# Kernel tuning notes

Hardware: AMD Instinct MI355X
Metric: run time of the kernel (lower is better)

The kernel has to match this reference:

```python
import jax, jax.numpy as jnp
import numpy as np

EPS = 1e-6
NUM_HEADS = 16


def _layer_norm(x, alpha, beta):
    # Custom LN: unbiased std, divides by (std + eps) -- matches source exactly.
    mean = jnp.mean(x, axis=-1, keepdims=True)
    std = jnp.std(x, axis=-1, keepdims=True, ddof=1)
    return alpha * (x - mean) / (std + EPS) + beta


def _mha(x, wq, bq, wk, bk, wv, bv, wo, bo):
    B, S, D = x.shape
    H = NUM_HEADS
    Dh = D // H
    q = (x @ wq.T + bq).reshape(B, S, H, Dh)
    k = (x @ wk.T + bk).reshape(B, S, H, Dh)
    v = (x @ wv.T + bv).reshape(B, S, H, Dh)
    scores = jnp.einsum('bqhd,bkhd->bhqk', q, k) / jnp.sqrt(jnp.float32(Dh)).astype(x.dtype)
    p = jax.nn.softmax(scores, axis=-1)
    out = jnp.einsum('bhqk,bkhd->bqhd', p, v).reshape(B, S, D)
    return out @ wo.T + bo


def _ffn(x, w1, b1, w2, b2):
    return jax.nn.relu(x @ w1.T + b1) @ w2.T + b2


def setup_inputs() -> dict:
    key = jax.random.key(0)
    ks = jax.random.split(key, 8)
    B, S, D, Hf = 8, 1024, 1024, 4096
    s = lambda d: 1.0 / np.sqrt(d)
    return {
        'x': jax.random.normal(ks[0], (B, S, D), jnp.float32),
        'src_mask': jnp.ones((B, 1, 1, S), jnp.int32),
        'wq': jax.random.normal(ks[1], (D, D), jnp.float32) * s(D),
        'bq': jnp.zeros((D,), jnp.float32),
        'wk': jax.random.normal(ks[2], (D, D), jnp.float32) * s(D),
        'bk': jnp.zeros((D,), jnp.float32),
        'wv': jax.random.normal(ks[3], (D, D), jnp.float32) * s(D),
        'bv': jnp.zeros((D,), jnp.float32),
        'wo': jax.random.normal(ks[4], (D, D), jnp.float32) * s(D),
        'bo': jnp.zeros((D,), jnp.float32),
        'w1': jax.random.normal(ks[5], (Hf, D), jnp.float32) * s(D),
        'b1': jnp.zeros((Hf,), jnp.float32),
        'w2': jax.random.normal(ks[6], (D, Hf), jnp.float32) * s(Hf),
        'b2': jnp.zeros((D,), jnp.float32),
        'alpha': jnp.ones((D,), jnp.float32),
        'beta': jnp.zeros((D,), jnp.float32),
    }


def reference(x, src_mask, wq, bq, wk, bk, wv, bv, wo, bo, w1, b1, w2, b2, alpha, beta):
    # src_mask is unused in the source's attention implementation (faithful).
    # Pre-LN residual block 1: attention (shared LN params alpha/beta).
    x = x + _mha(_layer_norm(x, alpha, beta), wq, bq, wk, bk, wv, bv, wo, bo)
    # Pre-LN residual block 2: feed-forward (same shared LN instance).
    x = x + _ffn(_layer_norm(x, alpha, beta), w1, b1, w2, b2)
    return x
```

## Files before the change

### kernel.cpp

```cpp
#include <hip/hip_runtime.h>
#include <hip/hip_bf16.h>
#include <stdint.h>

typedef __bf16 bf16;
typedef __attribute__((ext_vector_type(8))) __bf16 bf16x8;
typedef __attribute__((ext_vector_type(4))) __bf16 bf16x4;
typedef __attribute__((ext_vector_type(4))) float floatx4;

typedef __attribute__((address_space(3))) uint32_t* lds_u32p;
typedef const __attribute__((address_space(1))) uint32_t* glb_u32p;

__device__ __forceinline__ void gload16(void* lds, const void* g) {
  __builtin_amdgcn_global_load_lds((glb_u32p)(uintptr_t)g,
                                   (lds_u32p)(uintptr_t)lds, 16, 0, 0);
}

__global__ __launch_bounds__(256) void detect_kernel(
    const unsigned short* __restrict__ xr, int* __restrict__ flag) {
  __shared__ int cnt;
  if (threadIdx.x == 0) cnt = 0;
  __syncthreads();
  int c = 0;
  for (int i = threadIdx.x; i < 8192; i += 256) {
    unsigned short e = (xr[i] >> 7) & 0xFF;
    if (e >= 0x90) ++c;
  }
  atomicAdd(&cnt, c);
  __syncthreads();
  if (threadIdx.x == 0) *flag = (cnt > 64) ? 1 : 0;
}

#define NCONV 14
struct ConvArgs {
  const void* src[NCONV];
  bf16* dst[NCONV];
  int nelem[NCONV];
  int bstart[NCONV + 1];
};

__global__ __launch_bounds__(256) void convert_kernel(ConvArgs a, const int* __restrict__ flag) {
  const int isf = *flag;
  const int bx = blockIdx.x;
  int t = 0;
  #pragma unroll
  for (int i = 1; i < NCONV; ++i)
    if (bx >= a.bstart[i]) t = i;
  const int base = (bx - a.bstart[t]) * 2048 + threadIdx.x * 8;
  if (base >= a.nelem[t]) return;
  if (isf) {
    const float* s = (const float*)a.src[t] + base;
    const float4 x0 = *reinterpret_cast<const float4*>(s);
    const float4 x1 = *reinterpret_cast<const float4*>(s + 4);
    bf16x8 o;
    o[0] = (bf16)x0.x; o[1] = (bf16)x0.y; o[2] = (bf16)x0.z; o[3] = (bf16)x0.w;
    o[4] = (bf16)x1.x; o[5] = (bf16)x1.y; o[6] = (bf16)x1.z; o[7] = (bf16)x1.w;
    *reinterpret_cast<bf16x8*>(a.dst[t] + base) = o;
  } else {
    *reinterpret_cast<bf16x8*>(a.dst[t] + base) =
        *reinterpret_cast<const bf16x8*>((const bf16*)a.src[t] + base);
  }
}

__global__ __launch_bounds__(256) void ln_kernel(
    const void* __restrict__ x, const bf16* __restrict__ alpha,
    const bf16* __restrict__ beta, bf16* __restrict__ y,
    const int* __restrict__ flag, int x_ext) {
  const int isf = *flag;
  const int row = blockIdx.x;
  const int tid = threadIdx.x;

  float v0, v1, v2, v3;
  if (x_ext && isf) {
    const float4 xv = *reinterpret_cast<const float4*>(
        (const float*)x + (size_t)row * 1024 + tid * 4);
    v0 = xv.x; v1 = xv.y; v2 = xv.z; v3 = xv.w;
  } else {
    const bf16x4 xv = *reinterpret_cast<const bf16x4*>(
        (const bf16*)x + (size_t)row * 1024 + tid * 4);
    v0 = (float)xv[0]; v1 = (float)xv[1]; v2 = (float)xv[2]; v3 = (float)xv[3];
  }
  float s = v0 + v1 + v2 + v3;
  float ss = v0 * v0 + v1 * v1 + v2 * v2 + v3 * v3;
  #pragma unroll
  for (int off = 32; off > 0; off >>= 1) {
    s += __shfl_down(s, off);
    ss += __shfl_down(ss, off);
  }
  __shared__ float red[8];
  __shared__ float s_mean, s_inv;
  const int w = tid >> 6, lane = tid & 63;
  if (lane == 0) { red[w] = s; red[4 + w] = ss; }
  __syncthreads();
  if (tid == 0) {
    float S = red[0] + red[1] + red[2] + red[3];
    float SS = red[4] + red[5] + red[6] + red[7];
    float mean = S * (1.0f / 1024.0f);
    float var = (SS - 1024.0f * mean * mean) * (1.0f / 1023.0f);
    var = fmaxf(var, 0.0f);
    s_mean = mean;
    s_inv = 1.0f / (sqrtf(var) + 1e-6f);
  }
  __syncthreads();
  const float mean = s_mean, inv = s_inv;
  const bf16x4 av = *reinterpret_cast<const bf16x4*>(alpha + tid * 4);
  const bf16x4 bv = *reinterpret_cast<const bf16x4*>(beta + tid * 4);
  bf16x4 out;
  out[0] = (bf16)((float)av[0] * (v0 - mean) * inv + (float)bv[0]);
  out[1] = (bf16)((float)av[1] * (v1 - mean) * inv + (float)bv[1]);
  out[2] = (bf16)((float)av[2] * (v2 - mean) * inv + (float)bv[2]);
  out[3] = (bf16)((float)av[3] * (v3 - mean) * inv + (float)bv[3]);
  *reinterpret_cast<bf16x4*>(y + (size_t)row * 1024 + tid * 4) = out;
}

template <bool RELU, bool RES>
__global__ __launch_bounds__(256) void gemm_bt(
    const bf16* __restrict__ A, const bf16* __restrict__ W,
    const bf16* __restrict__ bias, const void* __restrict__ res,
    void* __restrict__ C, int M, int N, int K,
    const int* __restrict__ flag, int res_ext, int out_ext, int row0) {
  __shared__ bf16 As[128 * 64];
  __shared__ bf16 Bs[128 * 64];
  const int isf = *flag;
  const int tid = threadIdx.x;
  const int m0 = blockIdx.x * 128, n0 = blockIdx.y * 128;
  const int wave = tid >> 6, lane = tid & 63;
  const int wm = (wave >> 1) * 64, wn = (wave & 1) * 64;
  const int lrow = lane & 15, quad = lane >> 4;

  const int srow = lane >> 3;
  const int gchunk = (lane & 7) ^ srow;
  const bf16* Ab = A + (size_t)m0 * K;
  const bf16* Wb = W + (size_t)n0 * K;

  floatx4 acc[4][4] = {};

  for (int k0 = 0; k0 < K; k0 += 64) {
    __syncthreads();
    #pragma unroll
    for (int t = 0; t < 4; ++t) {
      const int r = t * 32 + wave * 8;
      gload16(&As[r * 64], Ab + (size_t)(r + srow) * K + k0 + gchunk * 8);
      gload16(&Bs[r * 64], Wb + (size_t)(r + srow) * K + k0 + gchunk * 8);
    }
    __syncthreads();

    #pragma unroll
    for (int ks = 0; ks < 2; ++ks) {
      const int cswz = ((ks * 4 + quad) ^ (lrow & 7)) * 8;
      bf16x8 af[4], bw[4];
      #pragma unroll
      for (int i = 0; i < 4; ++i) {
        af[i] = *reinterpret_cast<const bf16x8*>(&As[(wm + i * 16 + lrow) * 64 + cswz]);
        bw[i] = *reinterpret_cast<const bf16x8*>(&Bs[(wn + i * 16 + lrow) * 64 + cswz]);
      }
      #pragma unroll
      for (int i = 0; i < 4; ++i)
        #pragma unroll
        for (int j = 0; j < 4; ++j)
          acc[i][j] = __builtin_amdgcn_mfma_f32_16x16x32_bf16(af[i], bw[j], acc[i][j], 0, 0, 0);
    }
  }

  #pragma unroll
  for (int j = 0; j < 4; ++j) {
    const int col = n0 + wn + j * 16 + lrow;
    const float bv = (float)bias[col];
    #pragma unroll
    for (int i = 0; i < 4; ++i) {
      #pragma unroll
      for (int r = 0; r < 4; ++r) {
        const int row = m0 + wm + i * 16 + quad * 4 + r;
        float v = acc[i][j][r] + bv;
        if (RELU) v = fmaxf(v, 0.0f);
        if (RES) {
          const size_t ridx = (size_t)row * N + col;
          v += (res_ext && isf) ? ((const float*)res)[ridx]
                                : (float)((const bf16*)res)[ridx];
        }
        const size_t oidx = (size_t)(row0 + row) * N + col;
        if (out_ext && isf) ((float*)C)[oidx] = v;
        else ((bf16*)C)[oidx] = (bf16)v;
      }
    }
  }
}

template <bool RELU, bool RES>
__global__ __launch_bounds__(256) void gemm_n64(
    const bf16* __restrict__ A, const bf16* __restrict__ W,
    const bf16* __restrict__ bias, const void* __restrict__ res,
    void* __restrict__ C, int M, int N, int K,
    const int* __restrict__ flag, int res_ext, int out_ext, int row0) {
  __shared__ bf16 As[128 * 64];
  __shared__ bf16 Bs[64 * 64];
  const int isf = *flag;
  const int tid = threadIdx.x;
  const int m0 = blockIdx.x * 128, n0 = blockIdx.y * 64;
  const int wave = tid >> 6, lane = tid & 63;
  const int wm = (wave >> 1) * 64, wn = (wave & 1) * 32;
  const int lrow = lane & 15, quad = lane >> 4;

  const int srow = lane >> 3;
  const int gchunk = (lane & 7) ^ srow;
  const bf16* Ab = A + (size_t)m0 * K;
  const bf16* Wb = W + (size_t)n0 * K;

  floatx4 acc[4][2] = {};

  for (int k0 = 0; k0 < K; k0 += 64) {
    __syncthreads();
    #pragma unroll
    for (int t = 0; t < 4; ++t) {
      const int r = t * 32 + wave * 8;
      gload16(&As[r * 64], Ab + (size_t)(r + srow) * K + k0 + gchunk * 8);
    }
    #pragma unroll
    for (int t = 0; t < 2; ++t) {
      const int r = t * 32 + wave * 8;
      gload16(&Bs[r * 64], Wb + (size_t)(r + srow) * K + k0 + gchunk * 8);
    }
    __syncthreads();

    #pragma unroll
    for (int ks = 0; ks < 2; ++ks) {
      const int cswz = ((ks * 4 + quad) ^ (lrow & 7)) * 8;
      bf16x8 af[4], bw[2];
      #pragma unroll
      for (int i = 0; i < 4; ++i)
        af[i] = *reinterpret_cast<const bf16x8*>(&As[(wm + i * 16 + lrow) * 64 + cswz]);
      #pragma unroll
      for (int j = 0; j < 2; ++j)
        bw[j] = *reinterpret_cast<const bf16x8*>(&Bs[(wn + j * 16 + lrow) * 64 + cswz]);
      #pragma unroll
      for (int i = 0; i < 4; ++i)
        #pragma unroll
        for (int j = 0; j < 2; ++j)
          acc[i][j] = __builtin_amdgcn_mfma_f32_16x16x32_bf16(af[i], bw[j], acc[i][j], 0, 0, 0);
    }
  }

  #pragma unroll
  for (int j = 0; j < 2; ++j) {
    const int col = n0 + wn + j * 16 + lrow;
    const float bv = (float)bias[col];
    #pragma unroll
    for (int i = 0; i < 4; ++i) {
      #pragma unroll
      for (int r = 0; r < 4; ++r) {
        const int row = m0 + wm + i * 16 + quad * 4 + r;
        float v = acc[i][j][r] + bv;
        if (RELU) v = fmaxf(v, 0.0f);
        if (RES) {
          const size_t ridx = (size_t)row * N + col;
          v += (res_ext && isf) ? ((const float*)res)[ridx]
                                : (float)((const bf16*)res)[ridx];
        }
        const size_t oidx = (size_t)(row0 + row) * N + col;
        if (out_ext && isf) ((float*)C)[oidx] = v;
        else ((bf16*)C)[oidx] = (bf16)v;
      }
    }
  }
}

__global__ __launch_bounds__(512, 2) void gemm_ffn1_256(
    const bf16* __restrict__ A, const bf16* __restrict__ W,
    const bf16* __restrict__ bias, bf16* __restrict__ C) {
  constexpr int K = 1024, N = 4096, NK = K / 64;
  __shared__ bf16 As[2][256 * 64];
  __shared__ bf16 Bs[2][256 * 64];
  const int tid = threadIdx.x;
  const int wave = tid >> 6, lane = tid & 63;
  const int m0 = blockIdx.x * 256, n0 = blockIdx.y * 256;
  const int wm = (wave >> 2) * 128;
  const int wn = (wave & 3) * 64;
  const int lrow = lane & 15, quad = lane >> 4;
  const int srow = lane >> 3;
  const int gchunk = (lane & 7) ^ srow;
  const bf16* Ab = A + (size_t)m0 * K;
  const bf16* Wb = W + (size_t)n0 * K;
  const int awr = wave * 32;

  floatx4 acc[8][4] = {};

  auto piece = [&](int kt, int nb, int p) {
    const bf16* G = (p < 2) ? Ab : Wb;
    bf16* L = (p < 2) ? &As[nb][0] : &Bs[nb][0];
    #pragma unroll
    for (int t = (p & 1) * 2; t < (p & 1) * 2 + 2; ++t) {
      const int r = awr + t * 8;
      gload16(L + r * 64, G + (size_t)(r + srow) * K + kt * 64 + gchunk * 8);
    }
  };

  piece(0, 0, 0); piece(0, 0, 1); piece(0, 0, 2); piece(0, 0, 3);

  for (int kt = 0; kt < NK; ++kt) {
    const int cur = kt & 1, nb = cur ^ 1;
    const bool pre = (kt + 1 < NK);

    __builtin_amdgcn_sched_barrier(0);
    __builtin_amdgcn_s_barrier();
    __builtin_amdgcn_sched_barrier(0);
    if (pre) {
      piece(kt + 1, nb, 0);
      asm volatile("s_waitcnt vmcnt(2)" ::: "memory");
    } else {
      asm volatile("s_waitcnt vmcnt(0)" ::: "memory");
    }
    __builtin_amdgcn_sched_barrier(0);
    __builtin_amdgcn_s_barrier();
    __builtin_amdgcn_sched_barrier(0);

    bf16x8 bw[4][2];
    #pragma unroll
    for (int j = 0; j < 4; ++j) {
      const int row = wn + j * 16 + lrow;
      #pragma unroll
      for (int ks = 0; ks < 2; ++ks) {
        const int c = (ks * 4 + quad) ^ (lrow & 7);
        bw[j][ks] = *reinterpret_cast<const bf16x8*>(&Bs[cur][row * 64 + c * 8]);
      }
    }
    #pragma unroll
    for (int p = 0; p < 4; ++p) {
      bf16x8 af[2][2];
      #pragma unroll
      for (int il = 0; il < 2; ++il) {
        const int row = wm + (p * 2 + il) * 16 + lrow;
        #pragma unroll
        for (int ks = 0; ks < 2; ++ks) {
          const int c = (ks * 4 + quad) ^ (lrow & 7);
          af[il][ks] = *reinterpret_cast<const bf16x8*>(&As[cur][row * 64 + c * 8]);
        }
      }
      if (pre && p < 3) piece(kt + 1, nb, p + 1);
      __builtin_amdgcn_s_setprio(1);
      #pragma unroll
      for (int il = 0; il < 2; ++il)
        #pragma unroll
        for (int j = 0; j < 4; ++j)
          #pragma unroll
          for (int ks = 0; ks < 2; ++ks)
            acc[p * 2 + il][j] = __builtin_amdgcn_mfma_f32_16x16x32_bf16(
                af[il][ks], bw[j][ks], acc[p * 2 + il][j], 0, 0, 0);
      __builtin_amdgcn_s_setprio(0);
    }
  }

  #pragma unroll
  for (int j = 0; j < 4; ++j) {
    const int col = n0 + wn + j * 16 + lrow;
    const float bv = (float)bias[col];
    #pragma unroll
    for (int i = 0; i < 8; ++i) {
      #pragma unroll
      for (int r = 0; r < 4; ++r) {
        const int row = m0 + wm + i * 16 + quad * 4 + r;
        C[(size_t)row * N + col] = (bf16)fmaxf(acc[i][j][r] + bv, 0.0f);
      }
    }
  }
}

__global__ __launch_bounds__(256) void gemm_qkv(
    const bf16* __restrict__ A,
    const bf16* __restrict__ Wq, const bf16* __restrict__ Wk, const bf16* __restrict__ Wv,
    const bf16* __restrict__ Bq, const bf16* __restrict__ Bk, const bf16* __restrict__ Bv,
    bf16* __restrict__ Oq, bf16* __restrict__ Ok, bf16* __restrict__ Ov) {
  const int z = blockIdx.z;
  const bf16* W = (z == 0) ? Wq : (z == 1) ? Wk : Wv;
  const bf16* bias = (z == 0) ? Bq : (z == 1) ? Bk : Bv;
  bf16* C = (z == 0) ? Oq : (z == 1) ? Ok : Ov;
  const int K = 1024, N = 1024;

  __shared__ bf16 As[128 * 64];
  __shared__ bf16 Bs[128 * 64];
  const int tid = threadIdx.x;
  const int m0 = blockIdx.x * 128, n0 = blockIdx.y * 128;
  const int wave = tid >> 6, lane = tid & 63;
  const int wm = (wave >> 1) * 64, wn = (wave & 1) * 64;
  const int lrow = lane & 15, quad = lane >> 4;

  const int srow = lane >> 3;
  const int gchunk = (lane & 7) ^ srow;
  const bf16* Ab = A + (size_t)m0 * K;
  const bf16* Wb = W + (size_t)n0 * K;

  floatx4 acc[4][4] = {};

  for (int k0 = 0; k0 < K; k0 += 64) {
    __syncthreads();
    #pragma unroll
    for (int t = 0; t < 4; ++t) {
      const int r = t * 32 + wave * 8;
      gload16(&As[r * 64], Ab + (size_t)(r + srow) * K + k0 + gchunk * 8);
      gload16(&Bs[r * 64], Wb + (size_t)(r + srow) * K + k0 + gchunk * 8);
    }
    __syncthreads();

    #pragma unroll
    for (int ks = 0; ks < 2; ++ks) {
      const int cswz = ((ks * 4 + quad) ^ (lrow & 7)) * 8;
      bf16x8 af[4], bw[4];
      #pragma unroll
      for (int i = 0; i < 4; ++i) {
        af[i] = *reinterpret_cast<const bf16x8*>(&As[(wm + i * 16 + lrow) * 64 + cswz]);
        bw[i] = *reinterpret_cast<const bf16x8*>(&Bs[(wn + i * 16 + lrow) * 64 + cswz]);
      }
      #pragma unroll
      for (int i = 0; i < 4; ++i)
        #pragma unroll
        for (int j = 0; j < 4; ++j)
          acc[i][j] = __builtin_amdgcn_mfma_f32_16x16x32_bf16(af[i], bw[j], acc[i][j], 0, 0, 0);
    }
  }

  #pragma unroll
  for (int j = 0; j < 4; ++j) {
    const int col = n0 + wn + j * 16 + lrow;
    const float bv = (float)bias[col];
    #pragma unroll
    for (int i = 0; i < 4; ++i) {
      #pragma unroll
      for (int r = 0; r < 4; ++r) {
        const int row = m0 + wm + i * 16 + quad * 4 + r;
        C[(size_t)row * N + col] = (bf16)(acc[i][j][r] + bv);
      }
    }
  }
}

__global__ __launch_bounds__(256) void attn_kernel(
    const bf16* __restrict__ Qg, const bf16* __restrict__ Kg,
    const bf16* __restrict__ Vg, bf16* __restrict__ Og) {
  __shared__ bf16 Ks[64][72];
  __shared__ bf16 Vts[64][72];
  __shared__ bf16 Ps[4][32][72];

  const int tid = threadIdx.x, wave = tid >> 6, lane = tid & 63;
  const int lrow = lane & 15, quad = lane >> 4;
  const int bq = blockIdx.x, h = blockIdx.y, b = blockIdx.z;
  const int q0 = bq * 128 + wave * 32;

  bf16x8 qa[2][2];
  #pragma unroll
  for (int t = 0; t < 2; ++t) {
    const bf16* qbase = Qg + (size_t)(b * 1024 + q0 + t * 16 + lrow) * 1024 + h * 64;
    qa[t][0] = *reinterpret_cast<const bf16x8*>(qbase + quad * 8);
    qa[t][1] = *reinterpret_cast<const bf16x8*>(qbase + 32 + quad * 8);
  }

  const int skp = tid >> 2, sdd = (tid & 3) * 16;
  const int vkp = tid & 63, vdg = wave * 16;

  floatx4 o[2][4] = {};
  float lsum[2][4] = {};

  for (int kc = 0; kc < 1024; kc += 64) {
    __syncthreads();
    {
      const bf16* ksrc = Kg + (size_t)(b * 1024 + kc + skp) * 1024 + h * 64 + sdd;
      *reinterpret_cast<bf16x8*>(&Ks[skp][sdd]) = *reinterpret_cast<const bf16x8*>(ksrc);
      *reinterpret_cast<bf16x8*>(&Ks[skp][sdd + 8]) = *reinterpret_cast<const bf16x8*>(ksrc + 8);

      const bf16* vsrc = Vg + (size_t)(b * 1024 + kc + vkp) * 1024 + h * 64 + vdg;
      bf16x8 v0 = *reinterpret_cast<const bf16x8*>(vsrc);
      bf16x8 v1 = *reinterpret_cast<const bf16x8*>(vsrc + 8);
      #pragma unroll
      for (int j = 0; j < 8; ++j) {
        Vts[vdg + j][vkp] = v0[j];
        Vts[vdg + 8 + j][vkp] = v1[j];
      }
    }
    __syncthreads();

    #pragma unroll
    for (int t = 0; t < 2; ++t) {
      floatx4 s[4] = {};
      #pragma unroll
      for (int kt = 0; kt < 4; ++kt) {
        bf16x8 kb0 = *reinterpret_cast<const bf16x8*>(&Ks[kt * 16 + lrow][quad * 8]);
        bf16x8 kb1 = *reinterpret_cast<const bf16x8*>(&Ks[kt * 16 + lrow][32 + quad * 8]);
        s[kt] = __builtin_amdgcn_mfma_f32_16x16x32_bf16(qa[t][0], kb0, s[kt], 0, 0, 0);
        s[kt] = __builtin_amdgcn_mfma_f32_16x16x32_bf16(qa[t][1], kb1, s[kt], 0, 0, 0);
      }
      #pragma unroll
      for (int r = 0; r < 4; ++r) {
        const float p0 = __expf(s[0][r] * 0.125f);
        const float p1 = __expf(s[1][r] * 0.125f);
        const float p2 = __expf(s[2][r] * 0.125f);
        const float p3 = __expf(s[3][r] * 0.125f);
        lsum[t][r] += (p0 + p1) + (p2 + p3);
        const int qr = t * 16 + quad * 4 + r;
        Ps[wave][qr][lrow] = (bf16)p0;
        Ps[wave][qr][16 + lrow] = (bf16)p1;
        Ps[wave][qr][32 + lrow] = (bf16)p2;
        Ps[wave][qr][48 + lrow] = (bf16)p3;
      }
    }

    __builtin_amdgcn_wave_barrier();

    #pragma unroll
    for (int t = 0; t < 2; ++t) {
      const bf16x8 pf0 = *reinterpret_cast<const bf16x8*>(&Ps[wave][t * 16 + lrow][quad * 8]);
      const bf16x8 pf1 = *reinterpret_cast<const bf16x8*>(&Ps[wave][t * 16 + lrow][32 + quad * 8]);
      #pragma unroll
      for (int j = 0; j < 4; ++j) {
        bf16x8 vb0 = *reinterpret_cast<const bf16x8*>(&Vts[j * 16 + lrow][quad * 8]);
        bf16x8 vb1 = *reinterpret_cast<const bf16x8*>(&Vts[j * 16 + lrow][32 + quad * 8]);
        o[t][j] = __builtin_amdgcn_mfma_f32_16x16x32_bf16(pf0, vb0, o[t][j], 0, 0, 0);
        o[t][j] = __builtin_amdgcn_mfma_f32_16x16x32_bf16(pf1, vb1, o[t][j], 0, 0, 0);
      }
    }
  }

  #pragma unroll
  for (int t = 0; t < 2; ++t) {
    #pragma unroll
    for (int r = 0; r < 4; ++r) {
      float l = lsum[t][r];
      #pragma unroll
      for (int off = 1; off < 16; off <<= 1) l += __shfl_xor(l, off);
      const float inv = 1.0f / l;
      const size_t qrow = (size_t)(b * 1024 + q0 + t * 16 + quad * 4 + r);
      #pragma unroll
      for (int j = 0; j < 4; ++j)
        Og[qrow * 1024 + h * 64 + j * 16 + lrow] = (bf16)(o[t][j][r] * inv);
    }
  }
}

extern "C" void kernel_launch(void* const* d_in, const int* in_sizes, int n_in,
                              void* d_out, int out_size, void* d_ws, size_t ws_size,
                              hipStream_t stream) {
  const void* p[16];
  {
    int j = 0;
    for (int i = 0; i < 16; ++i) {
      if (i == 1) {
        if (j < n_in && in_sizes[j] == 8192) p[i] = d_in[j++];
        else p[i] = nullptr;
        continue;
      }
      p[i] = (j < n_in) ? d_in[j++] : nullptr;
    }
  }
  const void* x = p[0];

  char* ws = (char*)d_ws;
  int* flag = (int*)ws;
  char* wsc = ws + 256;

  const int wsz[NCONV] = {1048576, 1048576, 1048576, 1048576, 4194304, 4194304,
                          1024, 1024, 1024, 1024, 4096, 1024, 1024, 1024};
  const int wsrc[NCONV] = {2, 4, 6, 8, 10, 12, 3, 5, 7, 9, 11, 13, 14, 15};
  ConvArgs ca;
  bf16* cptr[NCONV];
  size_t off = 0;
  int bacc = 0;
  for (int i = 0; i < NCONV; ++i) {
    cptr[i] = (bf16*)(wsc + off);
    off += (size_t)wsz[i] * sizeof(bf16);
    ca.src[i] = p[wsrc[i]];
    ca.dst[i] = cptr[i];
    ca.nelem[i] = wsz[i];
    ca.bstart[i] = bacc;
    bacc += (wsz[i] + 2047) / 2048;
  }
  ca.bstart[NCONV] = bacc;
  const bf16 *wq_c = cptr[0], *wk_c = cptr[1], *wv_c = cptr[2], *wo_c = cptr[3];
  const bf16 *w1_c = cptr[4], *w2_c = cptr[5];
  const bf16 *bq_c = cptr[6], *bk_c = cptr[7], *bv_c = cptr[8], *bo_c = cptr[9];
  const bf16 *b1_c = cptr[10], *b2_c = cptr[11], *al_c = cptr[12], *be_c = cptr[13];

  char* base = wsc + ((off + 255) & ~(size_t)255);
  const size_t SZ = (size_t)8192 * 1024 * sizeof(bf16);
  bf16* s1 = (bf16*)(base);
  bf16* s0 = (bf16*)(base + SZ);
  bf16* s2 = (bf16*)(base + 2 * SZ);
  bf16* s3 = (bf16*)(base + 3 * SZ);
  bf16* Kb = (bf16*)d_out;

  const int M = 8192, D = 1024, HF = 4096;

  detect_kernel<<<1, 256, 0, stream>>>((const unsigned short*)x, flag);
  convert_kernel<<<bacc, 256, 0, stream>>>(ca, flag);
  ln_kernel<<<8192, 256, 0, stream>>>(x, al_c, be_c, s0, flag, 1);
  gemm_qkv<<<dim3(M / 128, D / 128, 3), 256, 0, stream>>>(
      s0, wq_c, wk_c, wv_c, bq_c, bk_c, bv_c, s1, Kb, s2);
  attn_kernel<<<dim3(8, 16, 8), 256, 0, stream>>>(s1, Kb, s2, s3);
  gemm_n64<false, true><<<dim3(M / 128, D / 64), 256, 0, stream>>>(
      s3, wo_c, bo_c, x, s1, M, D, D, flag, 1, 0, 0);
  ln_kernel<<<8192, 256, 0, stream>>>(s1, al_c, be_c, s0, flag, 0);

  const size_t used = (size_t)(base - ws) + 4 * SZ;
  if (ws_size >= used + (size_t)M * HF * sizeof(bf16)) {
    bf16* Hf = (bf16*)(base + 4 * SZ);
    gemm_ffn1_256<<<dim3(M / 256, HF / 256), 512, 0, stream>>>(s0, w1_c, b1_c, Hf);
    gemm_n64<false, true><<<dim3(M / 128, D / 64), 256, 0, stream>>>(
        Hf, w2_c, b2_c, s1, d_out, M, D, HF, flag, 0, 1, 0);
  } else {
    bf16* H = s2;
    for (int hh = 0; hh < 2; ++hh) {
      const size_t ro = (size_t)hh * 4096 * 1024;
      gemm_bt<true, false><<<dim3(32, 32), 256, 0, stream>>>(
          s0 + ro, w1_c, b1_c, nullptr, H, 4096, HF, D, flag, 0, 0, 0);
      gemm_n64<false, true><<<dim3(32, D / 64), 256, 0, stream>>>(
          H, w2_c, b2_c, s1 + ro, d_out, 4096, D, HF, flag, 0, 1, hh * 4096);
    }
  }
}
```

Before: 495.6 us.

## Use double-buffered 256-row pipelined GEMMs for QKV, out-proj and FFN2

```diff
diff --git a/kernel.cpp b/kernel.cpp
--- a/kernel.cpp
+++ b/kernel.cpp
@@ -363,69 +363,225 @@
   }
 }
 
-__global__ __launch_bounds__(256) void gemm_qkv(
-    const bf16* __restrict__ A,
-    const bf16* __restrict__ Wq, const bf16* __restrict__ Wk, const bf16* __restrict__ Wv,
-    const bf16* __restrict__ Bq, const bf16* __restrict__ Bk, const bf16* __restrict__ Bv,
+__global__ __launch_bounds__(512, 2) void gemm_qkv256(
+    const bf16* __restrict__ A, const bf16* __restrict__ W,
+    const bf16* __restrict__ bias,
     bf16* __restrict__ Oq, bf16* __restrict__ Ok, bf16* __restrict__ Ov) {
-  const int z = blockIdx.z;
-  const bf16* W = (z == 0) ? Wq : (z == 1) ? Wk : Wv;
-  const bf16* bias = (z == 0) ? Bq : (z == 1) ? Bk : Bv;
-  bf16* C = (z == 0) ? Oq : (z == 1) ? Ok : Ov;
-  const int K = 1024, N = 1024;
-
-  __shared__ bf16 As[128 * 64];
-  __shared__ bf16 Bs[128 * 64];
+  constexpr int K = 1024, NK = K / 64;
+  __shared__ bf16 As[2][256 * 64];
+  __shared__ bf16 Bs[2][256 * 64];
   const int tid = threadIdx.x;
-  const int m0 = blockIdx.x * 128, n0 = blockIdx.y * 128;
   const int wave = tid >> 6, lane = tid & 63;
-  const int wm = (wave >> 1) * 64, wn = (wave & 1) * 64;
+  const int m0 = blockIdx.x * 256, n0 = blockIdx.y * 256;
+  const int wm = (wave >> 2) * 128;
+  const int wn = (wave & 3) * 64;
   const int lrow = lane & 15, quad = lane >> 4;
-
   const int srow = lane >> 3;
   const int gchunk = (lane & 7) ^ srow;
   const bf16* Ab = A + (size_t)m0 * K;
   const bf16* Wb = W + (size_t)n0 * K;
-
-  floatx4 acc[4][4] = {};
-
-  for (int k0 = 0; k0 < K; k0 += 64) {
-    __syncthreads();
-    #pragma unroll
-    for (int t = 0; t < 4; ++t) {
-      const int r = t * 32 + wave * 8;
-      gload16(&As[r * 64], Ab + (size_t)(r + srow) * K + k0 + gchunk * 8);
-      gload16(&Bs[r * 64], Wb + (size_t)(r + srow) * K + k0 + gchunk * 8);
-    }
-    __syncthreads();
-
-    #pragma unroll
-    for (int ks = 0; ks < 2; ++ks) {
-      const int cswz = ((ks * 4 + quad) ^ (lrow & 7)) * 8;
-      bf16x8 af[4], bw[4];
-      #pragma unroll
-      for (int i = 0; i < 4; ++i) {
-        af[i] = *reinterpret_cast<const bf16x8*>(&As[(wm + i * 16 + lrow) * 64 + cswz]);
-        bw[i] = *reinterpret_cast<const bf16x8*>(&Bs[(wn + i * 16 + lrow) * 64 + cswz]);
-      }
-      #pragma unroll
-      for (int i = 0; i < 4; ++i)
+  const int awr = wave * 32;
+
+  floatx4 acc[8][4] = {};
+
+  auto piece = [&](int kt, int nb, int p) {
+    const bf16* G = (p < 2) ? Ab : Wb;
+    bf16* L = (p < 2) ? &As[nb][0] : &Bs[nb][0];
+    #pragma unroll
+    for (int t = (p & 1) * 2; t < (p & 1) * 2 + 2; ++t) {
+      const int r = awr + t * 8;
+      gload16(L + r * 64, G + (size_t)(r + srow) * K + kt * 64 + gchunk * 8);
+    }
+  };
+
+  piece(0, 0, 0); piece(0, 0, 1); piece(0, 0, 2); piece(0, 0, 3);
+
+  for (int kt = 0; kt < NK; ++kt) {
+    const int cur = kt & 1, nb = cur ^ 1;
+    const bool pre = (kt + 1 < NK);
+
+    __builtin_amdgcn_sched_barrier(0);
+    __builtin_amdgcn_s_barrier();
+    __builtin_amdgcn_sched_barrier(0);
+    if (pre) {
+      piece(kt + 1, nb, 0);
+      asm volatile("s_waitcnt vmcnt(2)" ::: "memory");
+    } else {
+      asm volatile("s_waitcnt vmcnt(0)" ::: "memory");
+    }
+    __builtin_amdgcn_sched_barrier(0);
+    __builtin_amdgcn_s_barrier();
+    __builtin_amdgcn_sched_barrier(0);
+
+    bf16x8 bw[4][2];
+    #pragma unroll
+    for (int j = 0; j < 4; ++j) {
+      const int row = wn + j * 16 + lrow;
+      #pragma unroll
+      for (int ks = 0; ks < 2; ++ks) {
+        const int c = (ks * 4 + quad) ^ (lrow & 7);
+        bw[j][ks] = *reinterpret_cast<const bf16x8*>(&Bs[cur][row * 64 + c * 8]);
+      }
+    }
+    #pragma unroll
+    for (int p = 0; p < 4; ++p) {
+      bf16x8 af[2][2];
+      #pragma unroll
+      for (int il = 0; il < 2; ++il) {
+        const int row = wm + (p * 2 + il) * 16 + lrow;
+        #pragma unroll
+        for (int ks = 0; ks < 2; ++ks) {
+          const int c = (ks * 4 + quad) ^ (lrow & 7);
+          af[il][ks] = *reinterpret_cast<const bf16x8*>(&As[cur][row * 64 + c * 8]);
+        }
+      }
+      if (pre && p < 3) piece(kt + 1, nb, p + 1);
+      __builtin_amdgcn_s_setprio(1);
+      #pragma unroll
+      for (int il = 0; il < 2; ++il)
         #pragma unroll
         for (int j = 0; j < 4; ++j)
-          acc[i][j] = __builtin_amdgcn_mfma_f32_16x16x32_bf16(af[i], bw[j], acc[i][j], 0, 0, 0);
+          #pragma unroll
+          for (int ks = 0; ks < 2; ++ks)
+            acc[p * 2 + il][j] = __builtin_amdgcn_mfma_f32_16x16x32_bf16(
+                af[il][ks], bw[j][ks], acc[p * 2 + il][j], 0, 0, 0);
+      __builtin_amdgcn_s_setprio(0);
     }
   }
 
   #pragma unroll
   for (int j = 0; j < 4; ++j) {
+    const int gcol = n0 + wn + j * 16 + lrow;
+    bf16* dst = (gcol < 1024) ? Oq : (gcol < 2048) ? Ok : Ov;
+    const int col = gcol & 1023;
+    const float bv = (float)bias[gcol];
+    #pragma unroll
+    for (int i = 0; i < 8; ++i) {
+      #pragma unroll
+      for (int r = 0; r < 4; ++r) {
+        const int row = m0 + wm + i * 16 + quad * 4 + r;
+        dst[(size_t)row * 1024 + col] = (bf16)(acc[i][j][r] + bv);
+      }
+    }
+  }
+}
+
+template <bool RELU, bool RES>
+__global__ __launch_bounds__(512, 2) void gemm_big(
+    const bf16* __restrict__ A, const bf16* __restrict__ W,
+    const bf16* __restrict__ bias, const void* __restrict__ res,
+    void* __restrict__ C, int M, int N, int K,
+    const int* __restrict__ flag, int res_ext, int out_ext) {
+  __shared__ bf16 As[2][256 * 64];
+  __shared__ bf16 Bs[2][128 * 64];
+  const int isf = *flag;
+  const int tid = threadIdx.x;
+  const int wave = tid >> 6, lane = tid & 63;
+  const int m0 = blockIdx.x * 256, n0 = blockIdx.y * 128;
+  const int wm = (wave >> 2) * 128;
+  const int wn = (wave & 3) * 32;
+  const int lrow = lane & 15, quad = lane >> 4;
+  const int srow = lane >> 3;
+  const int gchunk = (lane & 7) ^ srow;
+  const bf16* Ab = A + (size_t)m0 * K;
+  const bf16* Wb = W + (size_t)n0 * K;
+  const int awr = wave * 32;
+  const int bwr = wave * 16;
+
+  floatx4 acc[8][2] = {};
+
+  auto piece = [&](int kt, int nb, int p) {
+    if (p < 2) {
+      const int base = awr + p * 16;
+      #pragma unroll
+      for (int t = 0; t < 2; ++t) {
+        const int r = base + t * 8;
+        gload16(&As[nb][r * 64], Ab + (size_t)(r + srow) * K + kt * 64 + gchunk * 8);
+      }
+    } else {
+      #pragma unroll
+      for (int t = 0; t < 2; ++t) {
+        const int r = bwr + t * 8;
+        gload16(&Bs[nb][r * 64], Wb + (size_t)(r + srow) * K + kt * 64 + gchunk * 8);
+      }
+    }
+  };
+
+  const int nk = K >> 6;
+  piece(0, 0, 0); piece(0, 0, 1); piece(0, 0, 2);
+
+  for (int kt = 0; kt < nk; ++kt) {
+    const int cur = kt & 1, nb = cur ^ 1;
+    const bool pre = (kt + 1 < nk);
+
+    __builtin_amdgcn_sched_barrier(0);
+    __builtin_amdgcn_s_barrier();
+    __builtin_amdgcn_sched_barrier(0);
+    if (pre) {
+      piece(kt + 1, nb, 0);
+      asm volatile("s_waitcnt vmcnt(2)" ::: "memory");
+    } else {
+      asm volatile("s_waitcnt vmcnt(0)" ::: "memory");
+    }
+    __builtin_amdgcn_sched_barrier(0);
+    __builtin_amdgcn_s_barrier();
+    __builtin_amdgcn_sched_barrier(0);
+
+    bf16x8 bw[2][2];
+    #pragma unroll
+    for (int j = 0; j < 2; ++j) {
+      const int row = wn + j * 16 + lrow;
+      #pragma unroll
+      for (int ks = 0; ks < 2; ++ks) {
+        const int c = (ks * 4 + quad) ^ (lrow & 7);
+        bw[j][ks] = *reinterpret_cast<const bf16x8*>(&Bs[cur][row * 64 + c * 8]);
+      }
+    }
+    #pragma unroll
+    for (int p = 0; p < 4; ++p) {
+      bf16x8 af[2][2];
+      #pragma unroll
+      for (int il = 0; il < 2; ++il) {
+        const int row = wm + (p * 2 + il) * 16 + lrow;
+        #pragma unroll
+        for (int ks = 0; ks < 2; ++ks) {
+          const int c = (ks * 4 + quad) ^ (lrow & 7);
+          af[il][ks] = *reinterpret_cast<const bf16x8*>(&As[cur][row * 64 + c * 8]);
+        }
+      }
+      if (pre && p < 2) piece(kt + 1, nb, p + 1);
+      __builtin_amdgcn_s_setprio(1);
+      #pragma unroll
+      for (int il = 0; il < 2; ++il)
+        #pragma unroll
+        for (int j = 0; j < 2; ++j)
+          #pragma unroll
+          for (int ks = 0; ks < 2; ++ks)
+            acc[p * 2 + il][j] = __builtin_amdgcn_mfma_f32_16x16x32_bf16(
+                af[il][ks], bw[j][ks], acc[p * 2 + il][j], 0, 0, 0);
+      __builtin_amdgcn_s_setprio(0);
+    }
+  }
+
+  #pragma unroll
+  for (int j = 0; j < 2; ++j) {
     const int col = n0 + wn + j * 16 + lrow;
     const float bv = (float)bias[col];
     #pragma unroll
-    for (int i = 0; i < 4; ++i) {
+    for (int i = 0; i < 8; ++i) {
       #pragma unroll
       for (int r = 0; r < 4; ++r) {
         const int row = m0 + wm + i * 16 + quad * 4 + r;
-        C[(size_t)row * N + col] = (bf16)(acc[i][j][r] + bv);
+        float v = acc[i][j][r] + bv;
+        if (RELU) v = fmaxf(v, 0.0f);
+        if (RES) {
+          const size_t ridx = (size_t)row * N + col;
+          v += (res_ext && isf) ? ((const float*)res)[ridx]
+                                : (float)((const bf16*)res)[ridx];
+        }
+        const size_t oidx = (size_t)row * N + col;
+        if (out_ext && isf) ((float*)C)[oidx] = v;
+        else ((bf16*)C)[oidx] = (bf16)v;
       }
     }
   }
@@ -570,9 +726,9 @@
     bacc += (wsz[i] + 2047) / 2048;
   }
   ca.bstart[NCONV] = bacc;
-  const bf16 *wq_c = cptr[0], *wk_c = cptr[1], *wv_c = cptr[2], *wo_c = cptr[3];
+  const bf16 *wq_c = cptr[0], *wo_c = cptr[3];
   const bf16 *w1_c = cptr[4], *w2_c = cptr[5];
-  const bf16 *bq_c = cptr[6], *bk_c = cptr[7], *bv_c = cptr[8], *bo_c = cptr[9];
+  const bf16 *bq_c = cptr[6], *bo_c = cptr[9];
   const bf16 *b1_c = cptr[10], *b2_c = cptr[11], *al_c = cptr[12], *be_c = cptr[13];
 
   char* base = wsc + ((off + 255) & ~(size_t)255);
@@ -588,19 +744,19 @@
   detect_kernel<<<1, 256, 0, stream>>>((const unsigned short*)x, flag);
   convert_kernel<<<bacc, 256, 0, stream>>>(ca, flag);
   ln_kernel<<<8192, 256, 0, stream>>>(x, al_c, be_c, s0, flag, 1);
-  gemm_qkv<<<dim3(M / 128, D / 128, 3), 256, 0, stream>>>(
-      s0, wq_c, wk_c, wv_c, bq_c, bk_c, bv_c, s1, Kb, s2);
+  gemm_qkv256<<<dim3(M / 256, 3072 / 256), 512, 0, stream>>>(
+      s0, wq_c, bq_c, s1, Kb, s2);
   attn_kernel<<<dim3(8, 16, 8), 256, 0, stream>>>(s1, Kb, s2, s3);
-  gemm_n64<false, true><<<dim3(M / 128, D / 64), 256, 0, stream>>>(
-      s3, wo_c, bo_c, x, s1, M, D, D, flag, 1, 0, 0);
+  gemm_big<false, true><<<dim3(M / 256, D / 128), 512, 0, stream>>>(
+      s3, wo_c, bo_c, x, s1, M, D, D, flag, 1, 0);
   ln_kernel<<<8192, 256, 0, stream>>>(s1, al_c, be_c, s0, flag, 0);
 
   const size_t used = (size_t)(base - ws) + 4 * SZ;
   if (ws_size >= used + (size_t)M * HF * sizeof(bf16)) {
     bf16* Hf = (bf16*)(base + 4 * SZ);
     gemm_ffn1_256<<<dim3(M / 256, HF / 256), 512, 0, stream>>>(s0, w1_c, b1_c, Hf);
-    gemm_n64<false, true><<<dim3(M / 128, D / 64), 256, 0, stream>>>(
-        Hf, w2_c, b2_c, s1, d_out, M, D, HF, flag, 0, 1, 0);
+    gemm_big<false, true><<<dim3(M / 256, D / 128), 512, 0, stream>>>(
+        Hf, w2_c, b2_c, s1, d_out, M, D, HF, flag, 0, 1);
   } else {
     bf16* H = s2;
     for (int hh = 0; hh < 2; ++hh) {
```

After: 480.7 us. 1.03x faster.
